# Optimization experiments

Hardware: AMD Instinct MI355X
Metric: run time of the kernel (lower is better)

The kernel has to match this reference:

```python
import jax, jax.numpy as jnp
import numpy as np

B, H, S, D = 2, 16, 2048, 128
BS = 128  # block_size
NB = S // BS  # num_blocks
SPARSITY_PROB = 0.5


def setup_inputs() -> dict:
    key = jax.random.key(0)
    kq, kk, kv, km = jax.random.split(key, 4)
    query = jax.random.normal(kq, (B, H, S, D), dtype=jnp.float32)
    k_ = jax.random.normal(kk, (B, H, S, D), dtype=jnp.float32)
    v_ = jax.random.normal(kv, (B, H, S, D), dtype=jnp.float32)
    # block pattern: rand < sparsity_prob, diagonal forced True (causal=False)
    block_mask = jax.random.uniform(km, (NB, NB)) < SPARSITY_PROB
    block_mask = block_mask | jnp.eye(NB, dtype=bool)
    return {"query": query, "key": k_, "value": v_,
            "block_mask": block_mask, "block_size": BS}


def reference(query, key, value, block_mask, block_size):
    b, h, s, d = query.shape
    nb = s // block_size
    scale = 1.0 / jnp.sqrt(jnp.float32(d))
    # reshape into blocks: (b, h, nb, bs, d)
    qb = query.reshape(b, h, nb, block_size, d)
    kb = key.reshape(b, h, nb, block_size, d)
    vb = value.reshape(b, h, nb, block_size, d)
    # per-(i,j)-block scores: (b, h, i, j, q, k)
    scores = jnp.einsum('bhiqd,bhjkd->bhijqk', qb, kb) * scale
    # IMPORTANT: softmax is taken independently within each block (axis=-1),
    # matching the original's per-block (non-merged) softmax.
    attn = jax.nn.softmax(scores, axis=-1)
    # zero out inactive blocks, then sum contributions over j
    attn = attn * block_mask[None, None, :, :, None, None].astype(attn.dtype)
    out = jnp.einsum('bhijqk,bhjkd->bhiqd', attn, vb)
    return out.reshape(b, h, s, d)
```

## Files before the change

### kernel.cpp

```cpp
#include <hip/hip_runtime.h>
#include <stdint.h>

#define CBDIM 256
#define WBDIM 256
#define DBDIM 512

typedef __attribute__((ext_vector_type(8))) short short8;
typedef __attribute__((ext_vector_type(4))) float f32x4;

__device__ __forceinline__ unsigned f2bf(float f) {
    union { float f; unsigned u; } a; a.f = f;
    unsigned r = a.u + 0x7fffu + ((a.u >> 16) & 1u);
    return (r >> 16) & 0xffffu;
}
__device__ __forceinline__ float f4e(float4 v, int e) {
    return e == 0 ? v.x : e == 1 ? v.y : e == 2 ? v.z : v.w;
}
__device__ __forceinline__ unsigned u4e(uint4 v, int e) {
    return e == 0 ? v.x : e == 1 ? v.y : e == 2 ? v.z : v.w;
}
__device__ __forceinline__ uint2 shfl_u2(uint2 v, int src) {
    uint2 r;
    r.x = (unsigned)__shfl((int)v.x, src);
    r.y = (unsigned)__shfl((int)v.y, src);
    return r;
}
__device__ __forceinline__ bool detect_bf16(const void* p) {
    unsigned w = ((const unsigned*)p)[threadIdx.x & 63];
    unsigned lo = w & 0xffffu, ex = (lo >> 7) & 0xffu;
    bool pl = (lo == 0u) || (ex >= 0x68u && ex <= 0x86u);
    return __popcll(__ballot(pl)) >= 40;
}
__device__ __forceinline__ void gload_lds16(const void* g, void* l) {
    __builtin_amdgcn_global_load_lds(
        (const __attribute__((address_space(1))) void*)g,
        (__attribute__((address_space(3))) void*)l, 16, 0, 0);
}

__global__ __launch_bounds__(CBDIM)
void convert_kswz(const void* __restrict__ src, uint4* __restrict__ dst, int nIds)
{
    bool isBf = detect_bf16(src);
    int stride = gridDim.x * CBDIM;
    for (int id = blockIdx.x * CBDIM + threadIdx.x; id < nIds; id += stride) {
        int lid = id & 2047, tt = id >> 11;
        int r = lid >> 4, c = (lid & 15) ^ (r & 7);
        size_t eo = (size_t)tt * 16384 + (size_t)r * 128 + c * 8;
        uint4 w;
        if (isBf) {
            w = *(const uint4*)((const unsigned short*)src + eo);
        } else {
            const float* p = (const float*)src + eo;
            float4 f0 = *(const float4*)p, f1 = *(const float4*)(p + 4);
            w.x = f2bf(f0.x) | (f2bf(f0.y) << 16);
            w.y = f2bf(f0.z) | (f2bf(f0.w) << 16);
            w.z = f2bf(f1.x) | (f2bf(f1.y) << 16);
            w.w = f2bf(f1.z) | (f2bf(f1.w) << 16);
        }
        dst[id] = w;
    }
}

__global__ __launch_bounds__(CBDIM)
void convert_vt(const void* __restrict__ src, uint4* __restrict__ dst,
                const unsigned char* __restrict__ Mb, int* __restrict__ order)
{
    __shared__ unsigned short lv[16384];
    const int tid = threadIdx.x, t = blockIdx.x;
    bool isBf = detect_bf16(src);

    if (t == 0 && tid < 64) {
        int tt = tid;
        unsigned mu = ((const unsigned*)Mb)[tt];
        bool maskByte = (__ballot((mu & 0xFFFFFF00u) != 0u) != 0ull);
        int cnt = 0;
        if (tt < 16)
            for (int j = 0; j < 16; ++j) {
                bool a = maskByte ? (Mb[tt * 16 + j] != 0)
                                  : (((const int*)Mb)[tt * 16 + j] != 0);
                cnt += a ? 1 : 0;
            }
        int rank = 0;
        for (int j = 0; j < 16; ++j) {
            int cj = __shfl(cnt, j);
            if (cj > cnt || (cj == cnt && j < tt)) ++rank;
        }
        if (tt < 16) order[rank] = tt;
    }

    size_t ebase = (size_t)t * 16384;
    if (isBf) {
#pragma unroll
        for (int it = 0; it < 8; ++it) {
            int id = it * CBDIM + tid;
            *(uint4*)&lv[id * 8] = ((const uint4*)src)[ebase / 8 + id];
        }
    } else {
#pragma unroll
        for (int it = 0; it < 16; ++it) {
            int f = it * CBDIM + tid;
            float4 v = ((const float4*)src)[ebase / 4 + f];
            uint2 pk;
            pk.x = f2bf(v.x) | (f2bf(v.y) << 16);
            pk.y = f2bf(v.z) | (f2bf(v.w) << 16);
            *(uint2*)&lv[f * 4] = pk;
        }
    }
    __syncthreads();
#pragma unroll
    for (int it = 0; it < 8; ++it) {
        int id = it * CBDIM + tid;
        int d = id >> 4, c = (id & 15) ^ (d & 7);
        const unsigned short* col = &lv[(size_t)(c * 8) * 128 + d];
        uint4 w;
        w.x = col[0]   | ((unsigned)col[128] << 16);
        w.y = col[256] | ((unsigned)col[384] << 16);
        w.z = col[512] | ((unsigned)col[640] << 16);
        w.w = col[768] | ((unsigned)col[896] << 16);
        dst[(size_t)t * 2048 + id] = w;
    }
}

template<bool QF32>
__device__ __forceinline__ void attn_core(const void* Qv, const uint4* Kw,
                                          const uint4* Vt, unsigned actm,
                                          void* Ov, char* ldsK, char* ldsV,
                                          int bh, int i)
{
    constexpr int S = 2048, D = 128;
    const int tid  = threadIdx.x;
    const int lane = tid & 63;
    const int wv   = tid >> 6;
    const int quad = lane >> 4;
    const int l16  = lane & 15;

    const int qb0 = wv * 32;
    const size_t qrowbase = ((size_t)bh * S + (size_t)i * 128) * D;

    short8 qf[2][4];
#pragma unroll
    for (int nt = 0; nt < 2; ++nt) {
        int qrow = qb0 + nt * 16 + l16;
#pragma unroll
        for (int ks = 0; ks < 4; ++ks) {
            int dof = ks * 32 + quad * 8;
            if constexpr (QF32) {
                const float* qp = (const float*)Qv + qrowbase + (size_t)qrow * D + dof;
                float4 f0 = *(const float4*)qp;
                float4 f1 = *(const float4*)(qp + 4);
                short8 v;
                v[0] = (short)f2bf(f0.x); v[1] = (short)f2bf(f0.y);
                v[2] = (short)f2bf(f0.z); v[3] = (short)f2bf(f0.w);
                v[4] = (short)f2bf(f1.x); v[5] = (short)f2bf(f1.y);
                v[6] = (short)f2bf(f1.z); v[7] = (short)f2bf(f1.w);
                qf[nt][ks] = v;
            } else {
                qf[nt][ks] = *(const short8*)((const unsigned short*)Qv
                              + qrowbase + (size_t)qrow * D + dof);
            }
        }
    }

    f32x4 accO[2][8];
#pragma unroll
    for (int a = 0; a < 2; ++a)
#pragma unroll
        for (int b = 0; b < 8; ++b)
            accO[a][b] = (f32x4){0.f, 0.f, 0.f, 0.f};

    const float C2 = 0.08838834764831845f * 1.44269504088896f;
    const int srcA = l16 + ((quad & 1) << 5);
    const int srcB = srcA + 16;
    const bool hiMs = (quad >> 1) != 0;

    unsigned m = actm;
    while (m) {
        int j = (int)__builtin_ctz(m); m &= m - 1;
        const uint4* kt = Kw + (size_t)(bh * 16 + j) * 2048;
        const uint4* vt = Vt + (size_t)(bh * 16 + j) * 2048;

        __syncthreads();

#pragma unroll
        for (int it = 0; it < 8; ++it) {
            int id = it * WBDIM + tid;
            int lo = (it * WBDIM + wv * 64) * 16;
            gload_lds16(kt + id, ldsK + lo);
            gload_lds16(vt + id, ldsV + lo);
        }
        asm volatile("s_waitcnt vmcnt(0)" ::: "memory");
        __syncthreads();

        f32x4 accS[2][8];
#pragma unroll
        for (int nt = 0; nt < 2; ++nt)
#pragma unroll
            for (int mt = 0; mt < 8; ++mt)
                accS[nt][mt] = (f32x4){0.f, 0.f, 0.f, 0.f};

#pragma unroll
        for (int mt = 0; mt < 8; ++mt) {
            int r = mt * 16 + l16;
            short8 kf[4];
#pragma unroll
            for (int ks = 0; ks < 4; ++ks) {
                int c = ks * 4 + quad;
                kf[ks] = *(const short8*)(ldsK + r * 256 + ((c ^ (r & 7)) << 4));
            }
            __builtin_amdgcn_s_setprio(1);
#pragma unroll
            for (int nt = 0; nt < 2; ++nt)
#pragma unroll
                for (int ks = 0; ks < 4; ++ks)
                    accS[nt][mt] = __builtin_amdgcn_mfma_f32_16x16x32_bf16(
                        kf[ks], qf[nt][ks], accS[nt][mt], 0, 0, 0);
            __builtin_amdgcn_s_setprio(0);
        }

        uint2 p2[2][8];
#pragma unroll
        for (int nt = 0; nt < 2; ++nt) {
            float ps[8];
#pragma unroll
            for (int mt = 0; mt < 8; ++mt) {
                f32x4 p;
#pragma unroll
                for (int rr = 0; rr < 4; ++rr)
                    p[rr] = exp2f(accS[nt][mt][rr] * C2);
                accS[nt][mt] = p;
                ps[mt] = (p[0] + p[1]) + (p[2] + p[3]);
            }
            float sum = ((ps[0] + ps[1]) + (ps[2] + ps[3]))
                      + ((ps[4] + ps[5]) + (ps[6] + ps[7]));
            sum += __shfl_xor(sum, 16);
            sum += __shfl_xor(sum, 32);
            float rinv = 1.0f / sum;
#pragma unroll
            for (int mt = 0; mt < 8; ++mt) {
                p2[nt][mt].x = f2bf(accS[nt][mt][0] * rinv)
                             | (f2bf(accS[nt][mt][1] * rinv) << 16);
                p2[nt][mt].y = f2bf(accS[nt][mt][2] * rinv)
                             | (f2bf(accS[nt][mt][3] * rinv) << 16);
            }
        }

#pragma unroll
        for (int ks = 0; ks < 4; ++ks) {
            short8 pf[2];
#pragma unroll
            for (int nt = 0; nt < 2; ++nt) {
                uint2 a0 = shfl_u2(p2[nt][2 * ks + 0], srcA);
                uint2 a1 = shfl_u2(p2[nt][2 * ks + 1], srcA);
                uint2 b0 = shfl_u2(p2[nt][2 * ks + 0], srcB);
                uint2 b1 = shfl_u2(p2[nt][2 * ks + 1], srcB);
                uint2 lo, hi;
                lo.x = hiMs ? a1.x : a0.x;  lo.y = hiMs ? a1.y : a0.y;
                hi.x = hiMs ? b1.x : b0.x;  hi.y = hiMs ? b1.y : b0.y;
                union { uint4 u; short8 s; } w;
                w.u.x = lo.x; w.u.y = lo.y; w.u.z = hi.x; w.u.w = hi.y;
                pf[nt] = w.s;
            }
            __builtin_amdgcn_s_setprio(1);
#pragma unroll
            for (int dt = 0; dt < 8; ++dt) {
                int d = dt * 16 + l16;
                int c = ks * 4 + quad;
                short8 vf = *(const short8*)(ldsV + d * 256 + ((c ^ (d & 7)) << 4));
                accO[0][dt] = __builtin_amdgcn_mfma_f32_16x16x32_bf16(
                    pf[0], vf, accO[0][dt], 0, 0, 0);
                accO[1][dt] = __builtin_amdgcn_mfma_f32_16x16x32_bf16(
                    pf[1], vf, accO[1][dt], 0, 0, 0);
            }
            __builtin_amdgcn_s_setprio(0);
        }
    }

#pragma unroll
    for (int mt = 0; mt < 2; ++mt)
#pragma unroll
        for (int rr = 0; rr < 4; ++rr) {
            int qrow = qb0 + mt * 16 + quad * 4 + rr;
#pragma unroll
            for (int nt = 0; nt < 8; ++nt) {
                size_t idx = qrowbase + (size_t)qrow * D + nt * 16 + l16;
                if constexpr (QF32)
                    ((float*)Ov)[idx] = accO[mt][nt][rr];
                else
                    ((unsigned short*)Ov)[idx] = (unsigned short)f2bf(accO[mt][nt][rr]);
            }
        }
}

__global__ __launch_bounds__(WBDIM, 2)
void attn_ws(const void* __restrict__ Q, const uint4* __restrict__ Kw,
             const uint4* __restrict__ Vt, const unsigned char* __restrict__ Mb,
             const int* __restrict__ order, void* __restrict__ O)
{
    __shared__ uint4 ldsK4[2048];
    __shared__ uint4 ldsV4[2048];
    int blk = blockIdx.x;
    int bh = ((blk >> 7) << 3) | (blk & 7);
    int slot = (blk >> 3) & 15;
    int i = order[(blk >> 8) ? (15 - slot) : slot];
    bool qBf = detect_bf16(Q);
    unsigned mu = ((const unsigned*)Mb)[threadIdx.x & 63];
    bool maskByte = (__ballot((mu & 0xFFFFFF00u) != 0u) != 0ull);
    unsigned actm = 0;
#pragma unroll
    for (int j = 0; j < 16; ++j) {
        bool a = maskByte ? (Mb[i * 16 + j] != 0)
                          : (((const int*)Mb)[i * 16 + j] != 0);
        actm |= (a ? 1u : 0u) << j;
    }
    if (qBf)
        attn_core<false>(Q, Kw, Vt, actm, O, (char*)ldsK4, (char*)ldsV4, bh, i);
    else
        attn_core<true>(Q, Kw, Vt, actm, O, (char*)ldsK4, (char*)ldsV4, bh, i);
}

template<bool QF32, bool KVF32>
__device__ __forceinline__ void attn_body(const void* Qv, const void* Kv,
                                          const void* Vv,
                                          const unsigned char* Mb, bool maskByte,
                                          void* Ov, char* ldsK, char* ldsV,
                                          int bh, int i)
{
    constexpr int S = 2048, D = 128;
    const int tid  = threadIdx.x;
    const int lane = tid & 63;
    const int wave = tid >> 6;
    const int quad = lane >> 4;
    const int l16  = lane & 15;

    const int qb0 = wave * 16;
    const size_t qrowbase = ((size_t)bh * S + (size_t)i * 128) * D;

    short8 qf[4];
    {
        int qrow = qb0 + l16;
#pragma unroll
        for (int ks = 0; ks < 4; ++ks) {
            int dof = ks * 32 + quad * 8;
            if constexpr (QF32) {
                const float* qp = (const float*)Qv + qrowbase + (size_t)qrow * D + dof;
                float4 f0 = *(const float4*)qp;
                float4 f1 = *(const float4*)(qp + 4);
                short8 v;
                v[0] = (short)f2bf(f0.x); v[1] = (short)f2bf(f0.y);
                v[2] = (short)f2bf(f0.z); v[3] = (short)f2bf(f0.w);
                v[4] = (short)f2bf(f1.x); v[5] = (short)f2bf(f1.y);
                v[6] = (short)f2bf(f1.z); v[7] = (short)f2bf(f1.w);
                qf[ks] = v;
            } else {
                qf[ks] = *(const short8*)((const unsigned short*)Qv
                          + qrowbase + (size_t)qrow * D + dof);
            }
        }
    }

    f32x4 accO[8];
#pragma unroll
    for (int b = 0; b < 8; ++b)
        accO[b] = (f32x4){0.f, 0.f, 0.f, 0.f};

    const float C2 = 0.08838834764831845f * 1.44269504088896f;
    const int srcA = l16 + ((quad & 1) << 5);
    const int srcB = srcA + 16;
    const bool hiMs = (quad >> 1) != 0;

    for (int j = 0; j < 16; ++j) {
        bool active = maskByte ? (Mb[i * 16 + j] != 0)
                               : (((const int*)Mb)[i * 16 + j] != 0);
        if (!active) continue;

        __syncthreads();
        const size_t kb = ((size_t)bh * S + (size_t)j * 128) * D;

        if constexpr (KVF32) {
#pragma unroll
            for (int it = 0; it < 8; ++it) {
                int f = it * DBDIM + tid;
                int r = f >> 5, c4 = f & 31;
                float4 v = ((const float4*)((const float*)Kv + kb))[f];
                uint2 pk;
                pk.x = f2bf(v.x) | (f2bf(v.y) << 16);
                pk.y = f2bf(v.z) | (f2bf(v.w) << 16);
                int ch = c4 >> 1;
                *(uint2*)(ldsK + r * 256 + ((ch ^ (r & 7)) << 4)
                          + ((c4 & 1) << 3)) = pk;
            }
        } else {
#pragma unroll
            for (int it = 0; it < 4; ++it) {
                int id = it * DBDIM + tid;
                int r = id >> 4, ch = id & 15;
                uint4 v = ((const uint4*)((const unsigned short*)Kv + kb))[id];
                *(uint4*)(ldsK + r * 256 + ((ch ^ (r & 7)) << 4)) = v;
            }
        }

        {
            int id = tid, pp = id & 31, dc = id >> 5;
            if constexpr (KVF32) {
                const float* vb = (const float*)Vv + kb + (size_t)(4 * pp) * D + dc * 8;
                float4 ra[4], rb[4];
#pragma unroll
                for (int r = 0; r < 4; ++r) {
                    ra[r] = *(const float4*)(vb + (size_t)r * D);
                    rb[r] = *(const float4*)(vb + (size_t)r * D + 4);
                }
#pragma unroll
                for (int e = 0; e < 8; ++e) {
                    float v0 = (e < 4) ? f4e(ra[0], e) : f4e(rb[0], e - 4);
                    float v1 = (e < 4) ? f4e(ra[1], e) : f4e(rb[1], e - 4);
                    float v2 = (e < 4) ? f4e(ra[2], e) : f4e(rb[2], e - 4);
                    float v3 = (e < 4) ? f4e(ra[3], e) : f4e(rb[3], e - 4);
                    uint2 pk;
                    pk.x = f2bf(v0) | (f2bf(v1) << 16);
                    pk.y = f2bf(v2) | (f2bf(v3) << 16);
                    int d = dc * 8 + e;
                    *(uint2*)(ldsV + d * 256 + (((pp >> 1) ^ (d & 7)) << 4)
                              + ((pp & 1) << 3)) = pk;
                }
            } else {
                const unsigned short* vb = (const unsigned short*)Vv + kb
                                           + (size_t)(4 * pp) * D + dc * 8;
                uint4 r0 = *(const uint4*)(vb);
                uint4 r1 = *(const uint4*)(vb + D);
                uint4 r2 = *(const uint4*)(vb + 2 * D);
                uint4 r3 = *(const uint4*)(vb + 3 * D);
#pragma unroll
                for (int e = 0; e < 8; ++e) {
                    unsigned h0 = u4e(r0, e >> 1), h1 = u4e(r1, e >> 1);
                    unsigned h2 = u4e(r2, e >> 1), h3 = u4e(r3, e >> 1);
                    if (e & 1) { h0 >>= 16; h1 >>= 16; h2 >>= 16; h3 >>= 16; }
                    uint2 pk;
                    pk.x = (h0 & 0xffffu) | (h1 << 16);
                    pk.y = (h2 & 0xffffu) | (h3 << 16);
                    int d = dc * 8 + e;
                    *(uint2*)(ldsV + d * 256 + (((pp >> 1) ^ (d & 7)) << 4)
                              + ((pp & 1) << 3)) = pk;
                }
            }
        }
        __syncthreads();

        f32x4 accS[8];
#pragma unroll
        for (int mt = 0; mt < 8; ++mt)
            accS[mt] = (f32x4){0.f, 0.f, 0.f, 0.f};

#pragma unroll
        for (int mt = 0; mt < 8; ++mt) {
            int r = mt * 16 + l16;
            short8 kf[4];
#pragma unroll
            for (int ks = 0; ks < 4; ++ks) {
                int c = ks * 4 + quad;
                kf[ks] = *(const short8*)(ldsK + r * 256 + ((c ^ (r & 7)) << 4));
            }
#pragma unroll
            for (int ks = 0; ks < 4; ++ks)
                accS[mt] = __builtin_amdgcn_mfma_f32_16x16x32_bf16(
                    kf[ks], qf[ks], accS[mt], 0, 0, 0);
        }

        float ps[8];
#pragma unroll
        for (int mt = 0; mt < 8; ++mt) {
            f32x4 p;
#pragma unroll
            for (int rr = 0; rr < 4; ++rr)
                p[rr] = exp2f(accS[mt][rr] * C2);
            accS[mt] = p;
            ps[mt] = (p[0] + p[1]) + (p[2] + p[3]);
        }
        float sum = ((ps[0] + ps[1]) + (ps[2] + ps[3]))
                  + ((ps[4] + ps[5]) + (ps[6] + ps[7]));
        sum += __shfl_xor(sum, 16);
        sum += __shfl_xor(sum, 32);
        float rinv = 1.0f / sum;

        uint2 p2[8];
#pragma unroll
        for (int mt = 0; mt < 8; ++mt) {
            p2[mt].x = f2bf(accS[mt][0] * rinv) | (f2bf(accS[mt][1] * rinv) << 16);
            p2[mt].y = f2bf(accS[mt][2] * rinv) | (f2bf(accS[mt][3] * rinv) << 16);
        }

#pragma unroll
        for (int ks = 0; ks < 4; ++ks) {
            short8 pf;
            {
                uint2 a0 = shfl_u2(p2[2 * ks + 0], srcA);
                uint2 a1 = shfl_u2(p2[2 * ks + 1], srcA);
                uint2 b0 = shfl_u2(p2[2 * ks + 0], srcB);
                uint2 b1 = shfl_u2(p2[2 * ks + 1], srcB);
                uint2 lo, hi;
                lo.x = hiMs ? a1.x : a0.x;  lo.y = hiMs ? a1.y : a0.y;
                hi.x = hiMs ? b1.x : b0.x;  hi.y = hiMs ? b1.y : b0.y;
                union { uint4 u; short8 s; } w;
                w.u.x = lo.x; w.u.y = lo.y; w.u.z = hi.x; w.u.w = hi.y;
                pf = w.s;
            }
#pragma unroll
            for (int dt = 0; dt < 8; ++dt) {
                int d = dt * 16 + l16;
                int c = ks * 4 + quad;
                short8 vf = *(const short8*)(ldsV + d * 256 + ((c ^ (d & 7)) << 4));
                accO[dt] = __builtin_amdgcn_mfma_f32_16x16x32_bf16(
                    pf, vf, accO[dt], 0, 0, 0);
            }
        }
    }

#pragma unroll
    for (int rr = 0; rr < 4; ++rr) {
        int qrow = qb0 + quad * 4 + rr;
#pragma unroll
        for (int dt = 0; dt < 8; ++dt) {
            size_t idx = qrowbase + (size_t)qrow * D + dt * 16 + l16;
            if constexpr (QF32)
                ((float*)Ov)[idx] = accO[dt][rr];
            else
                ((unsigned short*)Ov)[idx] = (unsigned short)f2bf(accO[dt][rr]);
        }
    }
}

__global__ __launch_bounds__(DBDIM, 4)
void attn_direct(const void* __restrict__ Q, const void* __restrict__ K,
                 const void* __restrict__ V,
                 const unsigned char* __restrict__ Mb, void* __restrict__ O)
{
    __shared__ uint4 ldsK4[2048];
    __shared__ uint4 ldsV4[2048];
    int blk = blockIdx.x;
    int bh = ((blk >> 7) << 3) | (blk & 7);
    int i  = (blk >> 3) & 15;
    bool qBf = detect_bf16(Q);
    unsigned mu = ((const unsigned*)Mb)[threadIdx.x & 63];
    bool maskByte = (__ballot((mu & 0xFFFFFF00u) != 0u) != 0ull);
    if (qBf)
        attn_body<false, false>(Q, K, V, Mb, maskByte, O,
                                (char*)ldsK4, (char*)ldsV4, bh, i);
    else
        attn_body<true, true>(Q, K, V, Mb, maskByte, O,
                              (char*)ldsK4, (char*)ldsV4, bh, i);
}

extern "C" void kernel_launch(void* const* d_in, const int* in_sizes, int n_in,
                              void* d_out, int out_size, void* d_ws, size_t ws_size,
                              hipStream_t stream) {
    const int NIDS = 512 * 2048;
    const size_t need = (size_t)NIDS * 16 * 2 + 256;
    if (ws_size >= need) {
        uint4* Kw = (uint4*)d_ws;
        uint4* Vt = Kw + NIDS;
        int* order = (int*)(Vt + NIDS);
        convert_kswz<<<1024, CBDIM, 0, stream>>>(d_in[1], Kw, NIDS);
        convert_vt<<<512, CBDIM, 0, stream>>>(d_in[2], Vt,
                                              (const unsigned char*)d_in[3], order);
        attn_ws<<<512, WBDIM, 0, stream>>>(d_in[0], Kw, Vt,
                                           (const unsigned char*)d_in[3],
                                           order, d_out);
    } else {
        attn_direct<<<512, DBDIM, 0, stream>>>(d_in[0], d_in[1], d_in[2],
                                               (const unsigned char*)d_in[3], d_out);
    }
}
```

Measured before the change: 216.7 us.

## Prefetch next K/V tiles during compute and use permlane swaps for P reshuffle

Measured after the change: 213.3 us. About the same (-1.6%).

```diff
diff --git a/kernel.cpp b/kernel.cpp
--- a/kernel.cpp
+++ b/kernel.cpp
@@ -4,6 +4,13 @@
 #define CBDIM 256
 #define WBDIM 256
 #define DBDIM 512
+
+#if __has_builtin(__builtin_amdgcn_permlane32_swap) && \
+    __has_builtin(__builtin_amdgcn_permlane16_swap)
+#define HAVE_PERMLANE_SWAP 1
+#else
+#define HAVE_PERMLANE_SWAP 0
+#endif
 
 typedef __attribute__((ext_vector_type(8))) short short8;
 typedef __attribute__((ext_vector_type(4))) float f32x4;
@@ -169,27 +176,30 @@
             accO[a][b] = (f32x4){0.f, 0.f, 0.f, 0.f};
 
     const float C2 = 0.08838834764831845f * 1.44269504088896f;
-    const int srcA = l16 + ((quad & 1) << 5);
-    const int srcB = srcA + 16;
-    const bool hiMs = (quad >> 1) != 0;
-
-    unsigned m = actm;
-    while (m) {
-        int j = (int)__builtin_ctz(m); m &= m - 1;
-        const uint4* kt = Kw + (size_t)(bh * 16 + j) * 2048;
-        const uint4* vt = Vt + (size_t)(bh * 16 + j) * 2048;
-
-        __syncthreads();
-
+
+    auto STAGE = [&](const uint4* t, char* lds) {
 #pragma unroll
         for (int it = 0; it < 8; ++it) {
             int id = it * WBDIM + tid;
             int lo = (it * WBDIM + wv * 64) * 16;
-            gload_lds16(kt + id, ldsK + lo);
-            gload_lds16(vt + id, ldsV + lo);
-        }
-        asm volatile("s_waitcnt vmcnt(0)" ::: "memory");
-        __syncthreads();
+            gload_lds16(t + id, lds + lo);
+        }
+        asm volatile("" ::: "memory");
+    };
+    auto ktile = [&](int jj) { return Kw + (size_t)(bh * 16 + jj) * 2048; };
+    auto vtile = [&](int jj) { return Vt + (size_t)(bh * 16 + jj) * 2048; };
+
+    int j = (int)__builtin_ctz(actm);
+    unsigned m = actm & (actm - 1);
+
+    STAGE(ktile(j), ldsK);
+    STAGE(vtile(j), ldsV);
+    asm volatile("s_waitcnt vmcnt(8)" ::: "memory");
+    __syncthreads();
+
+    while (true) {
+        int jn = m ? (int)__builtin_ctz(m) : -1;
+        if (jn >= 0) m &= m - 1;
 
         f32x4 accS[2][8];
 #pragma unroll
@@ -244,11 +254,29 @@
             }
         }
 
+        asm volatile("s_waitcnt vmcnt(0)" ::: "memory");
+        __syncthreads();
+        if (jn >= 0) STAGE(ktile(jn), ldsK);
+
 #pragma unroll
         for (int ks = 0; ks < 4; ++ks) {
             short8 pf[2];
 #pragma unroll
             for (int nt = 0; nt < 2; ++nt) {
+#if HAVE_PERMLANE_SWAP
+                unsigned ax = p2[nt][2 * ks + 0].x, ay = p2[nt][2 * ks + 0].y;
+                unsigned bx = p2[nt][2 * ks + 1].x, by = p2[nt][2 * ks + 1].y;
+                auto rx = __builtin_amdgcn_permlane32_swap(ax, bx, false, false);
+                auto ry = __builtin_amdgcn_permlane32_swap(ay, by, false, false);
+                auto sx = __builtin_amdgcn_permlane16_swap(rx[0], rx[1], false, false);
+                auto sy = __builtin_amdgcn_permlane16_swap(ry[0], ry[1], false, false);
+                union { uint4 u; short8 s; } w;
+                w.u.x = sx[0]; w.u.y = sy[0]; w.u.z = sx[1]; w.u.w = sy[1];
+                pf[nt] = w.s;
+#else
+                const int srcA = l16 + ((quad & 1) << 5);
+                const int srcB = srcA + 16;
+                const bool hiMs = (quad >> 1) != 0;
                 uint2 a0 = shfl_u2(p2[nt][2 * ks + 0], srcA);
                 uint2 a1 = shfl_u2(p2[nt][2 * ks + 1], srcA);
                 uint2 b0 = shfl_u2(p2[nt][2 * ks + 0], srcB);
@@ -259,6 +287,7 @@
                 union { uint4 u; short8 s; } w;
                 w.u.x = lo.x; w.u.y = lo.y; w.u.z = hi.x; w.u.w = hi.y;
                 pf[nt] = w.s;
+#endif
             }
             __builtin_amdgcn_s_setprio(1);
 #pragma unroll
@@ -273,6 +302,13 @@
             }
             __builtin_amdgcn_s_setprio(0);
         }
+
+        if (jn < 0) break;
+        __syncthreads();
+        STAGE(vtile(jn), ldsV);
+        asm volatile("s_waitcnt vmcnt(8)" ::: "memory");
+        __syncthreads();
+        j = jn;
     }
 
 #pragma unroll
```
